# Performance work log

Measured on AMD Instinct MI355X. Metric: run time of the kernel, lower is better.

## Reference

```python
import jax, jax.numpy as jnp
from jax import lax
import numpy as np

W = 64          # net_width
NITER = 10
THRESH = 1e-3
MSTEP = 1.0


def setup_inputs() -> dict:
    key = jax.random.key(0)
    ks = jax.random.split(key, 10)
    B, Nh, DIM = 8, 16384, 1024
    eye = jnp.eye(W, dtype=jnp.float32)
    return {
        'y_re': jax.random.normal(ks[0], (B, 1, Nh), jnp.float32),
        'y_im': jax.random.normal(ks[1], (B, 1, Nh), jnp.float32),
        'H_re': jax.random.normal(ks[2], (32768, DIM), jnp.float32) / np.sqrt(DIM),
        'H_im': jax.random.normal(ks[3], (32768, DIM), jnp.float32) / np.sqrt(DIM),
        # torch inits: estep.weight=I, estep.bias=0, update.weight=I, memory.weight=1e-6*I;
        # add small perturbations so the math is non-degenerate.
        'estep_w': eye + 0.05 * jax.random.normal(ks[4], (W, W), jnp.float32),
        'estep_b': jnp.zeros((W,), jnp.float32),
        'update_w': eye + 0.05 * jax.random.normal(ks[5], (W, W), jnp.float32),
        'update_b': 0.02 * jax.random.normal(ks[6], (W,), jnp.float32),
        'memory_w': 1e-6 * eye + 0.01 * jax.random.normal(ks[7], (W, W), jnp.float32),
        'memory_b': 0.02 * jax.random.normal(ks[8], (W,), jnp.float32),
    }


def _forward(y_re, y_im, H_re, H_im, estep_w, estep_b, update_w, update_b, memory_w, memory_b):
    y = (y_re + 1j * y_im).astype(jnp.complex64)          # [B,1,Nh]
    y = jnp.concatenate([y, jnp.conj(y)], axis=2)         # [B,1,N]
    H = (H_re + 1j * H_im).astype(jnp.complex64)          # [N,DIM]
    B, N = y.shape[0], y.shape[2]
    DIM = H.shape[1]
    nb = N // W
    Hb = H.reshape(nb, W, DIM)                            # [nb,W,DIM]
    yb = y.reshape(B, nb, W).transpose(1, 0, 2)[:, :, None, :]  # [nb,B,1,W]

    x0 = jnp.zeros((B, 1, DIM), jnp.complex64)
    tau0 = jnp.ones((nb, B, 1, W), jnp.float32)

    def block_step(xk, blk):
        H_i, y_i, tau_i = blk                              # [W,DIM], [B,1,W], [B,1,W]
        zk = jnp.einsum('bod,wd->bow', xk, H_i)            # [B,1,W] complex
        r = y_i - zk
        a2 = jnp.abs(r) ** 2                               # [B,1,W] float32
        # expectation_step: xt / std(xt) (torch.std = unbiased, global)
        xt = a2 / jnp.std(a2, ddof=1)
        ht = jax.nn.sigmoid(xt @ estep_w.T + estep_b)
        tau_new = jax.nn.relu(ht @ update_w.T + update_b + tau_i @ memory_w.T + memory_b)
        sigma2 = jnp.mean(a2, axis=2, keepdims=True)       # [B,1,1]
        residual = MSTEP * r * tau_new / sigma2            # complex
        xk = xk + jnp.einsum('bow,wd->bod', residual, jnp.conj(H_i)) / (W * DIM)
        return xk, tau_new

    def iteration(carry, _):
        xk, tau = carry
        xk, tau_new = lax.scan(block_step, xk, (Hb, yb, tau))  # sequential over blocks
        # soft threshold: sgn(x) * relu(|x| - threshold * max|x|)
        ax = jnp.abs(xk)
        m = jnp.max(ax)
        sgn = jnp.where(ax > 0, xk / jnp.where(ax > 0, ax, 1.0), 0.0 + 0.0j)
        xk = sgn * jax.nn.relu(ax - THRESH * m)
        return (xk, tau_new), None

    (xk, tau), _ = lax.scan(iteration, (x0, tau0), None, length=NITER)
    tau_out = tau[:, :, 0, :].transpose(1, 0, 2)           # [B,nb,W]
    return jnp.real(xk), tau_out


def reference(y_re, y_im, H_re, H_im, estep_w, estep_b, update_w, update_b, memory_w, memory_b):
    return _forward(y_re, y_im, H_re, H_im, estep_w, estep_b,
                    update_w, update_b, memory_w, memory_b)
```

## Files before the change

### kernel.cpp

```cpp
#include <hip/hip_runtime.h>
#include <math.h>

#define NT  256
#define NWG 64
#define SCOPE_AG __HIP_MEMORY_SCOPE_AGENT
typedef unsigned long long ull;

__device__ __forceinline__ float ld_f(const float* p) {
    return __hip_atomic_load(p, __ATOMIC_RELAXED, SCOPE_AG);
}
__device__ __forceinline__ void st_f(float* p, float v) {
    __hip_atomic_store(p, v, __ATOMIC_RELAXED, SCOPE_AG);
}
__device__ __forceinline__ unsigned ld_u(const unsigned* p) {
    return __hip_atomic_load(p, __ATOMIC_RELAXED, SCOPE_AG);
}
__device__ __forceinline__ void st_u(unsigned* p, unsigned v) {
    __hip_atomic_store(p, v, __ATOMIC_RELAXED, SCOPE_AG);
}
__device__ __forceinline__ void st_u_rel(unsigned* p, unsigned v) {
    __hip_atomic_store(p, v, __ATOMIC_RELEASE, SCOPE_AG);
}
__device__ __forceinline__ ull ld_u64(const ull* p) {
    return __hip_atomic_load(p, __ATOMIC_RELAXED, SCOPE_AG);
}
__device__ __forceinline__ void st_u64(ull* p, ull v) {
    __hip_atomic_store(p, v, __ATOMIC_RELAXED, SCOPE_AG);
}

__device__ __forceinline__ unsigned tagf(float v, unsigned tg) {
    return (__float_as_uint(v) & 0xFFFFFF00u) | tg;
}
__device__ __forceinline__ ull pack2(float lo, float hi, unsigned tg) {
    return ((ull)tagf(hi, tg) << 32) | (ull)tagf(lo, tg);
}

__device__ __forceinline__ float wsum64(float v) {
    #pragma unroll
    for (int m = 1; m < 64; m <<= 1) v += __shfl_xor(v, m);
    return v;
}
__device__ __forceinline__ float wmax64(float v) {
    #pragma unroll
    for (int m = 1; m < 64; m <<= 1) v = fmaxf(v, __shfl_xor(v, m));
    return v;
}


__launch_bounds__(NT, 1)
__global__ void robii_kernel(
    const float* __restrict__ y_re, const float* __restrict__ y_im,
    const float* __restrict__ H_re, const float* __restrict__ H_im,
    const float* __restrict__ estep_w, const float* __restrict__ estep_b,
    const float* __restrict__ update_w, const float* __restrict__ update_b,
    const float* __restrict__ memory_w, const float* __restrict__ memory_b,
    float* __restrict__ out, float* __restrict__ ws)
{
    __shared__ float wTe[4096], wTu[4096], wTm[4096];
    __shared__ float be[64], bu[64], bm[64];
    __shared__ float a2s[512];
    __shared__ float redl[8];
    __shared__ float gmax[1];
    __shared__ float2 rown[64];
    __shared__ float xts[64], hts[64], taurow[64];
    __shared__ float2 resid[64];
    __shared__ float2 cpartC[4][32][4];
    __shared__ float2 x_l[128];

    float* mpartf = (float*)cpartC;

    const int g = blockIdx.x, t = threadIdx.x;
    const int c = g & 7;
    const int b = g >> 3;
    const int lane = t & 63, wv = t >> 6;
    const int sub = t & 31;
    const int rbase = t >> 5;

    ull*      partuw = (ull*)ws;
    float*    tauws  = ws + 16384;
    unsigned* pm_u   = (unsigned*)(ws + 278528);

    for (int i = t; i < 4096; i += NT) {
        int j = i >> 6, k = i & 63;
        wTe[k * 64 + j] = estep_w[i];
        wTu[k * 64 + j] = update_w[i];
        wTm[k * 64 + j] = memory_w[i];
    }
    if (t < 64) { be[t] = estep_b[t]; bu[t] = update_b[t]; bm[t] = memory_b[t]; taurow[t] = 1.0f; }
    if (t < 128) x_l[t] = make_float2(0.0f, 0.0f);
    for (int i = t; i < 4096; i += NT) st_f(&tauws[g * 4096 + i], 1.0f);

    __syncthreads();
    if (t == 0) st_u_rel(&pm_u[g], tagf(1.0f, 255u));
    if (t < 64) {
        while ((ld_u(&pm_u[t]) & 0xFFu) != 255u) __builtin_amdgcn_s_sleep(1);
    }
    __builtin_amdgcn_fence(__ATOMIC_ACQUIRE, "agent");
    __syncthreads();

    const size_t hcol = (size_t)c * 128 + (size_t)sub * 4;

    float4 hAre[8], hAim[8], hBre[8], hBim[8];

#define PREF(DRE, DIM_, BLKN) do {                                                   \
        const float* _pr = H_re + ((size_t)(BLKN) * 64 + rbase) * 1024 + hcol;       \
        const float* _pi = H_im + ((size_t)(BLKN) * 64 + rbase) * 1024 + hcol;       \
        _Pragma("unroll")                                                            \
        for (int _j = 0; _j < 8; ++_j) {                                             \
            DRE[_j]  = *(const float4*)(_pr + (size_t)_j * 8192);                    \
            DIM_[_j] = *(const float4*)(_pi + (size_t)_j * 8192);                    \
        }                                                                            \
    } while (0)

    PREF(hAre, hAim, 0);

#define STEP(BLK, CRE, CIM, NRE, NIM) do {                                           \
        const int blk = (BLK);                                                       \
        const int par = blk & 1;                                                     \
        const unsigned tg = (unsigned)(iter * 512 + blk + 1) & 0xFFu;                \
        __syncthreads();                               \
           \
               \
        float2 xr0 = x_l[sub * 4 + 0], xr1 = x_l[sub * 4 + 1];                       \
        float2 xr2 = x_l[sub * 4 + 2], xr3 = x_l[sub * 4 + 3];                       \
        _Pragma("unroll")                                                            \
        for (int j = 0; j < 8; ++j) {                                                \
            float4 hr = CRE[j], hi = CIM[j];                                         \
            float sr, si;                                                            \
            sr  = xr0.x * hr.x - xr0.y * hi.x;  si  = xr0.x * hi.x + xr0.y * hr.x;   \
            sr += xr1.x * hr.y - xr1.y * hi.y;  si += xr1.x * hi.y + xr1.y * hr.y;   \
            sr += xr2.x * hr.z - xr2.y * hi.z;  si += xr2.x * hi.z + xr2.y * hr.z;   \
            sr += xr3.x * hr.w - xr3.y * hi.w;  si += xr3.x * hi.w + xr3.y * hr.w;   \
            _Pragma("unroll")                                                        \
            for (int m = 1; m < 32; m <<= 1) {                                       \
                sr += __shfl_xor(sr, m); si += __shfl_xor(si, m);                    \
            }                                                                        \
            if (sub == 0)                                                            \
                st_u64(&partuw[(size_t)par * 4096 + (b * 64 + rbase + 8 * j) * 8 + c], \
                       pack2(sr, si, tg));                                           \
        }                                                                            \
                     \
        PREF(NRE, NIM, ((blk + 1) & 511));                                           \
        float tau_nxt = 0.0f;                                                        \
        if (t < 64) tau_nxt = ld_f(&tauws[(((blk + 1) & 511) * 8 + b) * 64 + t]);    \
        float yAr, yAi, yBr, yBi;                                                    \
        {                                                                            \
            int b1 = t >> 6, w1 = t & 63, n1 = blk * 64 + w1;                        \
            if (n1 < 16384) { yAr = y_re[b1 * 16384 + n1];         yAi = y_im[b1 * 16384 + n1]; } \
            else            { yAr = y_re[b1 * 16384 + n1 - 16384]; yAi = -y_im[b1 * 16384 + n1 - 16384]; } \
            int i2 = t + 256;                                                        \
            int b2 = i2 >> 6, w2 = i2 & 63, n2 = blk * 64 + w2;                      \
            if (n2 < 16384) { yBr = y_re[b2 * 16384 + n2];         yBi = y_im[b2 * 16384 + n2]; } \
            else            { yBr = y_re[b2 * 16384 + n2 - 16384]; yBi = -y_im[b2 * 16384 + n2 - 16384]; } \
        }                                                                            \
         \
        _Pragma("unroll")                                                            \
        for (int e = 0; e < 2; ++e) {                                                \
            int idx = t + e * 256;                                                   \
            const ull* pb = partuw + (size_t)par * 4096 + (size_t)idx * 8;           \
            ull v0, v1, v2, v3, v4, v5, v6, v7;                                      \
            bool ok = false;                                                         \
            while (!ok) {                                                            \
                v0 = ld_u64(pb + 0); v1 = ld_u64(pb + 1);                            \
                v2 = ld_u64(pb + 2); v3 = ld_u64(pb + 3);                            \
                v4 = ld_u64(pb + 4); v5 = ld_u64(pb + 5);                            \
                v6 = ld_u64(pb + 6); v7 = ld_u64(pb + 7);                            \
                unsigned m01 = ((unsigned)v0 & 0xFFu) ^ tg;                          \
                m01 |= ((unsigned)(v0 >> 32) & 0xFFu) ^ tg;                          \
                m01 |= ((unsigned)v1 & 0xFFu) ^ tg;                                  \
                m01 |= ((unsigned)(v1 >> 32) & 0xFFu) ^ tg;                          \
                m01 |= ((unsigned)v2 & 0xFFu) ^ tg;                                  \
                m01 |= ((unsigned)(v2 >> 32) & 0xFFu) ^ tg;                          \
                m01 |= ((unsigned)v3 & 0xFFu) ^ tg;                                  \
                m01 |= ((unsigned)(v3 >> 32) & 0xFFu) ^ tg;                          \
                m01 |= ((unsigned)v4 & 0xFFu) ^ tg;                                  \
                m01 |= ((unsigned)(v4 >> 32) & 0xFFu) ^ tg;                          \
                m01 |= ((unsigned)v5 & 0xFFu) ^ tg;                                  \
                m01 |= ((unsigned)(v5 >> 32) & 0xFFu) ^ tg;                          \
                m01 |= ((unsigned)v6 & 0xFFu) ^ tg;                                  \
                m01 |= ((unsigned)(v6 >> 32) & 0xFFu) ^ tg;                          \
                m01 |= ((unsigned)v7 & 0xFFu) ^ tg;                                  \
                m01 |= ((unsigned)(v7 >> 32) & 0xFFu) ^ tg;                          \
                ok = (m01 == 0u);                                                    \
                if (!ok) __builtin_amdgcn_s_sleep(1);                                \
            }                                                                        \
            float zr = __uint_as_float((unsigned)v0) + __uint_as_float((unsigned)v1) \
                     + __uint_as_float((unsigned)v2) + __uint_as_float((unsigned)v3) \
                     + __uint_as_float((unsigned)v4) + __uint_as_float((unsigned)v5) \
                     + __uint_as_float((unsigned)v6) + __uint_as_float((unsigned)v7);\
            float zi = __uint_as_float((unsigned)(v0 >> 32)) + __uint_as_float((unsigned)(v1 >> 32)) \
                     + __uint_as_float((unsigned)(v2 >> 32)) + __uint_as_float((unsigned)(v3 >> 32)) \
                     + __uint_as_float((unsigned)(v4 >> 32)) + __uint_as_float((unsigned)(v5 >> 32)) \
                     + __uint_as_float((unsigned)(v6 >> 32)) + __uint_as_float((unsigned)(v7 >> 32));\
            float rr = ((e == 0) ? yAr : yBr) - zr;                                  \
            float ri = ((e == 0) ? yAi : yBi) - zi;                                  \
            a2s[idx] = rr * rr + ri * ri;                                            \
            int b1 = idx >> 6, w = idx & 63;                                         \
            if (b1 == b) rown[w] = make_float2(rr, ri);                              \
        }                                                                            \
        __syncthreads();                                                             \
                                       \
        float va = a2s[t] + a2s[t + 256];                                            \
        float s_ = wsum64(va);                                                       \
        if (lane == 0) redl[wv] = s_;                                                \
        __syncthreads();                                                             \
        float mean = (redl[0] + redl[1] + redl[2] + redl[3]) * (1.0f / 512.0f);      \
        float d0 = a2s[t] - mean, d1 = a2s[t + 256] - mean;                          \
        float s2_ = wsum64(d0 * d0 + d1 * d1);                                       \
        float sg  = wsum64(a2s[b * 64 + lane]) * (1.0f / 64.0f);                     \
        if (lane == 0) redl[4 + wv] = s2_;                                           \
        __syncthreads();                                                             \
        float stdv = sqrtf((redl[4] + redl[5] + redl[6] + redl[7]) * (1.0f / 511.0f)); \
        if (t < 64) xts[t] = a2s[b * 64 + t] / stdv;                                 \
        __syncthreads();                                                             \
                                \
        {                                                                            \
            int j = t & 63, q = t >> 6;                                              \
            float acc = 0.0f;                                                        \
            _Pragma("unroll")                                                        \
            for (int k16 = 0; k16 < 16; ++k16) {                                     \
                int k = q * 16 + k16;                                                \
                acc += wTe[k * 64 + j] * xts[k];                                     \
            }                                                                        \
            mpartf[q * 64 + j] = acc;                                                \
        }                                                                            \
        __syncthreads();                                                             \
        if (t < 64) {                                                                \
            float acc = be[t] + mpartf[t] + mpartf[64 + t] + mpartf[128 + t] + mpartf[192 + t]; \
            hts[t] = 1.0f / (1.0f + expf(-acc));                                     \
        }                                                                            \
        __syncthreads();                                                             \
                          \
        {                                                                            \
            int j = t & 63, q = t >> 6;                                              \
            float acc = 0.0f;                                                        \
            _Pragma("unroll")                                                        \
            for (int k16 = 0; k16 < 16; ++k16) {                                     \
                int k = q * 16 + k16;                                                \
                acc += wTu[k * 64 + j] * hts[k] + wTm[k * 64 + j] * taurow[k];       \
            }                                                                        \
            mpartf[q * 64 + j] = acc;                                                \
        }                                                                            \
        __syncthreads();                                                             \
        if (t < 64) {                                                                \
            float tn = bu[t] + bm[t] + mpartf[t] + mpartf[64 + t] + mpartf[128 + t] + mpartf[192 + t]; \
            tn = fmaxf(tn, 0.0f);                                                    \
            if (c == 0) st_f(&tauws[(blk * 8 + b) * 64 + t], tn);                    \
            float2 rv = rown[t];                                                     \
            float scl = tn / sg;                                                     \
            resid[t] = make_float2(rv.x * scl, rv.y * scl);                          \
        }                                                                            \
        __syncthreads();                                                             \
            \
        float2 ac0 = make_float2(0.f, 0.f), ac1 = make_float2(0.f, 0.f);             \
        float2 ac2 = make_float2(0.f, 0.f), ac3 = make_float2(0.f, 0.f);             \
        _Pragma("unroll")                                                            \
        for (int j = 0; j < 8; ++j) {                                                \
            float2 rs = resid[rbase + 8 * j];                                        \
            float4 hr = CRE[j], hi = CIM[j];                                         \
            ac0.x += rs.x * hr.x + rs.y * hi.x;  ac0.y += rs.y * hr.x - rs.x * hi.x; \
            ac1.x += rs.x * hr.y + rs.y * hi.y;  ac1.y += rs.y * hr.y - rs.x * hi.y; \
            ac2.x += rs.x * hr.z + rs.y * hi.z;  ac2.y += rs.y * hr.z - rs.x * hi.z; \
            ac3.x += rs.x * hr.w + rs.y * hi.w;  ac3.y += rs.y * hr.w - rs.x * hi.w; \
        }                                                                            \
        ac0.x += __shfl_xor(ac0.x, 32); ac0.y += __shfl_xor(ac0.y, 32);              \
        ac1.x += __shfl_xor(ac1.x, 32); ac1.y += __shfl_xor(ac1.y, 32);              \
        ac2.x += __shfl_xor(ac2.x, 32); ac2.y += __shfl_xor(ac2.y, 32);              \
        ac3.x += __shfl_xor(ac3.x, 32); ac3.y += __shfl_xor(ac3.y, 32);              \
        if ((t & 32) == 0) {                                                         \
            cpartC[wv][sub][0] = ac0; cpartC[wv][sub][1] = ac1;                      \
            cpartC[wv][sub][2] = ac2; cpartC[wv][sub][3] = ac3;                      \
        }                                                                            \
        if (t < 64) taurow[t] = tau_nxt;                  \
        __syncthreads();                                                             \
        if (t < 128) {                                                               \
            int sl = t >> 2, kk = t & 3;                                             \
            float2 s0 = cpartC[0][sl][kk], s1 = cpartC[1][sl][kk];                   \
            float2 s2 = cpartC[2][sl][kk], s3 = cpartC[3][sl][kk];                   \
            float2 xv = x_l[t];                                                      \
            xv.x += (s0.x + s1.x + s2.x + s3.x) * (1.0f / 65536.0f);                 \
            xv.y += (s0.y + s1.y + s2.y + s3.y) * (1.0f / 65536.0f);                 \
            x_l[t] = xv;                                                             \
        }                                                                            \
    } while (0)

    #pragma unroll 1
    for (int iter = 0; iter < 10; ++iter) {
        #pragma unroll 1
        for (int blk2 = 0; blk2 < 512; blk2 += 2) {
            STEP(blk2,     hAre, hAim, hBre, hBim);
            STEP(blk2 + 1, hBre, hBim, hAre, hAim);
        }

        const unsigned itg = (unsigned)(iter + 1);
        float lm = 0.0f;
        if (t < 128) { float2 xv = x_l[t]; lm = sqrtf(xv.x * xv.x + xv.y * xv.y); }
        lm = wmax64(lm);
        if (lane == 0) redl[wv] = lm;
        __syncthreads();
        if (t == 0)
            st_u_rel(&pm_u[g], tagf(fmaxf(fmaxf(redl[0], redl[1]), fmaxf(redl[2], redl[3])), itg));
        float pv = 0.0f;
        if (t < 64) {
            unsigned u;
            for (;;) {
                u = ld_u(&pm_u[t]);
                if ((u & 0xFFu) == itg) break;
                __builtin_amdgcn_s_sleep(1);
            }
            pv = __uint_as_float(u);
        }
        __builtin_amdgcn_fence(__ATOMIC_ACQUIRE, "agent");
        pv = wmax64(pv);
        if (t == 0) gmax[0] = pv;
        __syncthreads();
        float m = gmax[0];
        if (t < 128) {
            float2 xv = x_l[t];
            float ax = sqrtf(xv.x * xv.x + xv.y * xv.y);
            float s = (ax > 0.0f) ? fmaxf(ax - 1e-3f * m, 0.0f) / ax : 0.0f;
            x_l[t] = make_float2(xv.x * s, xv.y * s);
        }
        __syncthreads();
    }

    if (t < 128) out[b * 1024 + c * 128 + t] = x_l[t].x;
    for (int i = g * 8; i < g * 8 + 8; ++i) {
        for (int idx = t; idx < 512; idx += NT) {
            int bb = idx >> 6, w = idx & 63;
            out[8192 + bb * 32768 + i * 64 + w] = ld_f(&tauws[(i * 8 + bb) * 64 + w]);
        }
    }
#undef STEP
#undef PREF
}

__global__ void robii_diag_kernel(float* out, int code) {
    int i = blockIdx.x * blockDim.x + threadIdx.x;
    if (i < 8192) out[i] = 1.0e6f * (float)(1 + code);
}

extern "C" void kernel_launch(void* const* d_in, const int* in_sizes, int n_in,
                              void* d_out, int out_size, void* d_ws, size_t ws_size,
                              hipStream_t stream) {
    (void)in_sizes; (void)n_in; (void)out_size; (void)ws_size;
    const float* y_re     = (const float*)d_in[0];
    const float* y_im     = (const float*)d_in[1];
    const float* H_re     = (const float*)d_in[2];
    const float* H_im     = (const float*)d_in[3];
    const float* estep_w  = (const float*)d_in[4];
    const float* estep_b  = (const float*)d_in[5];
    const float* update_w = (const float*)d_in[6];
    const float* update_b = (const float*)d_in[7];
    const float* memory_w = (const float*)d_in[8];
    const float* memory_b = (const float*)d_in[9];
    float* outp = (float*)d_out;
    float* wsp  = (float*)d_ws;

    hipLaunchKernelGGL(robii_kernel, dim3(NWG), dim3(NT), 0, stream,
                       y_re, y_im, H_re, H_im, estep_w, estep_b,
                       update_w, update_b, memory_w, memory_b, outp, wsp);
    hipError_t e = hipGetLastError();
    if (e != hipSuccess) {
        hipLaunchKernelGGL(robii_diag_kernel, dim3(32), dim3(256), 0, stream,
                           outp, (int)e);
    }
}
```

Measured before the change: 37.74 ms.

## Process block pairs per step using precomputed bf16 cross-block Gram matrices

```diff
diff --git a/kernel.cpp b/kernel.cpp
--- a/kernel.cpp
+++ b/kernel.cpp
@@ -15,9 +15,6 @@
 __device__ __forceinline__ unsigned ld_u(const unsigned* p) {
     return __hip_atomic_load(p, __ATOMIC_RELAXED, SCOPE_AG);
 }
-__device__ __forceinline__ void st_u(unsigned* p, unsigned v) {
-    __hip_atomic_store(p, v, __ATOMIC_RELAXED, SCOPE_AG);
-}
 __device__ __forceinline__ void st_u_rel(unsigned* p, unsigned v) {
     __hip_atomic_store(p, v, __ATOMIC_RELEASE, SCOPE_AG);
 }
@@ -34,6 +31,13 @@
 __device__ __forceinline__ ull pack2(float lo, float hi, unsigned tg) {
     return ((ull)tagf(hi, tg) << 32) | (ull)tagf(lo, tg);
 }
+__device__ __forceinline__ unsigned bf16pack(float even, float odd) {
+    unsigned ua = __float_as_uint(even); ua += 0x7FFFu + ((ua >> 16) & 1u);
+    unsigned ub = __float_as_uint(odd);  ub += 0x7FFFu + ((ub >> 16) & 1u);
+    return (ua >> 16) | (ub & 0xFFFF0000u);
+}
+__device__ __forceinline__ float bf16lo(unsigned w) { return __uint_as_float(w << 16); }
+__device__ __forceinline__ float bf16hi(unsigned w) { return __uint_as_float(w & 0xFFFF0000u); }
 
 __device__ __forceinline__ float wsum64(float v) {
     #pragma unroll
@@ -46,9 +50,402 @@
     return v;
 }
 
+#define GRAM_WS_BYTES 5374208ull
+#define PART_OFF 1048576
+#define TAU_OFF  1081344
+#define PM_OFF   1343488
+
+__launch_bounds__(256, 1)
+__global__ void gram_kernel(const float* __restrict__ H_re, const float* __restrict__ H_im,
+                            unsigned* __restrict__ Ttab) {
+    __shared__ float2 Als[64 * 65];
+    __shared__ float2 Bls[64 * 65];
+    const int i = blockIdx.x;
+    const int t = threadIdx.x;
+    const int w = t & 63;
+    const int wp0 = (t >> 6) * 16;
+    const size_t baseA = (size_t)(2 * i) * 65536;
+    const size_t baseB = baseA + 65536;
+    float2 acc[16];
+    #pragma unroll
+    for (int s = 0; s < 16; ++s) acc[s] = make_float2(0.0f, 0.0f);
+
+    for (int ch = 0; ch < 16; ++ch) {
+        __syncthreads();
+        for (int k = t; k < 4096; k += 256) {
+            int r = k >> 6, d = k & 63;
+            size_t off = (size_t)r * 1024 + ch * 64 + d;
+            Als[r * 65 + d] = make_float2(H_re[baseA + off], H_im[baseA + off]);
+            Bls[r * 65 + d] = make_float2(H_re[baseB + off], H_im[baseB + off]);
+        }
+        __syncthreads();
+        #pragma unroll
+        for (int s = 0; s < 16; ++s) {
+            int wp = wp0 + s;
+            float ar = 0.0f, ai = 0.0f;
+            #pragma unroll 8
+            for (int d = 0; d < 64; ++d) {
+                float2 a = Als[wp * 65 + d];
+                float2 bb = Bls[w * 65 + d];
+                ar += a.x * bb.x + a.y * bb.y;
+                ai += a.x * bb.y - a.y * bb.x;
+            }
+            acc[s].x += ar; acc[s].y += ai;
+        }
+    }
+    #pragma unroll
+    for (int s = 0; s < 16; ++s)
+        Ttab[(size_t)i * 4096 + w * 64 + (wp0 + s)] = bf16pack(acc[s].x, acc[s].y);
+}
 
 __launch_bounds__(NT, 1)
-__global__ void robii_kernel(
+__global__ void robii_gram(
+    const float* __restrict__ y_re, const float* __restrict__ y_im,
+    const float* __restrict__ H_re, const float* __restrict__ H_im,
+    const float* __restrict__ estep_w, const float* __restrict__ estep_b,
+    const float* __restrict__ update_w, const float* __restrict__ update_b,
+    const float* __restrict__ memory_w, const float* __restrict__ memory_b,
+    float* __restrict__ out, float* __restrict__ ws)
+{
+    __shared__ float wTe[4096], wTu[4096], wTm[4096];
+    __shared__ float be[64], bu[64], bm[64];
+    __shared__ float a2s[512], xts[512], htl[512];
+    __shared__ float redl[8], sgls[8], gmax[1];
+    __shared__ float tauls[1024];
+    __shared__ float2 resA[512], resB[512];
+    __shared__ unsigned Tls[4160];
+    __shared__ float2 cpartC[4][32][4];
+    __shared__ float2 x_l[128];
+
+    const int g = blockIdx.x, t = threadIdx.x;
+    const int c = g & 7;
+    const int b = g >> 3;
+    const int lane = t & 63, wv = t >> 6;
+    const int sub = t & 31;
+    const int rbase = t >> 5;
+
+    unsigned* Ttab  = (unsigned*)ws;
+    ull*      partuw = (ull*)(ws + PART_OFF);
+    float*    tauws  = ws + TAU_OFF;
+    unsigned* pm_u   = (unsigned*)(ws + PM_OFF);
+
+    for (int i = t; i < 4096; i += NT) {
+        int j = i >> 6, k = i & 63;
+        wTe[k * 64 + j] = estep_w[i];
+        wTu[k * 64 + j] = update_w[i];
+        wTm[k * 64 + j] = memory_w[i];
+    }
+    if (t < 64) { be[t] = estep_b[t]; bu[t] = update_b[t]; bm[t] = memory_b[t]; }
+    if (t < 128) x_l[t] = make_float2(0.0f, 0.0f);
+    for (int i = t; i < 1024; i += NT) tauls[i] = 1.0f;
+    for (int i = t; i < 4096; i += NT) st_f(&tauws[g * 4096 + i], 1.0f);
+
+    __syncthreads();
+    if (t == 0) st_u_rel(&pm_u[g], tagf(1.0f, 255u));
+    if (t < 64) {
+        while ((ld_u(&pm_u[t]) & 0xFFu) != 255u) __builtin_amdgcn_s_sleep(1);
+    }
+    __builtin_amdgcn_fence(__ATOMIC_ACQUIRE, "agent");
+    __syncthreads();
+
+    const size_t hcol = (size_t)c * 128 + (size_t)sub * 4;
+    float4 hAre[8], hAim[8], hBre[8], hBim[8];
+    float4 hCre[8], hCim[8], hDre[8], hDim[8];
+
+#define PREF(DRE, DIM_, BLKN) do {                                                   \
+        const float* _pr = H_re + ((size_t)(BLKN) * 64 + rbase) * 1024 + hcol;       \
+        const float* _pi = H_im + ((size_t)(BLKN) * 64 + rbase) * 1024 + hcol;       \
+        _Pragma("unroll")                                                            \
+        for (int _j = 0; _j < 8; ++_j) {                                             \
+            DRE[_j]  = *(const float4*)(_pr + (size_t)_j * 8192);                    \
+            DIM_[_j] = *(const float4*)(_pi + (size_t)_j * 8192);                    \
+        }                                                                            \
+    } while (0)
+
+    PREF(hAre, hAim, 0);
+    PREF(hBre, hBim, 1);
+
+#define TCHK(V) (((((unsigned)(V)) & 0xFFu) ^ tg) | ((((unsigned)((V) >> 32)) & 0xFFu) ^ tg))
+
+#define WSTEP(WN, PRE_, PIM_, QRE_, QIM_, NRE_, NIM_, N2RE_, N2IM_) do {             \
+        const int wn_ = (WN);                                                        \
+        const int par = wn_ & 1;                                                     \
+        const int K0 = 2 * wn_;                                                      \
+        const unsigned tg = (unsigned)(iter * 256 + wn_) & 0xFFu;                    \
+        __syncthreads();                                                             \
+            \
+        float2 xr0 = x_l[sub * 4 + 0], xr1 = x_l[sub * 4 + 1];                       \
+        float2 xr2 = x_l[sub * 4 + 2], xr3 = x_l[sub * 4 + 3];                       \
+        _Pragma("unroll")                                                            \
+        for (int j = 0; j < 8; ++j) {                                                \
+            float4 pr = PRE_[j], pi = PIM_[j], qr = QRE_[j], qi = QIM_[j];           \
+            float sr, si, ur, ui;                                                    \
+            sr  = xr0.x*pr.x - xr0.y*pi.x;  si  = xr0.x*pi.x + xr0.y*pr.x;           \
+            sr += xr1.x*pr.y - xr1.y*pi.y;  si += xr1.x*pi.y + xr1.y*pr.y;           \
+            sr += xr2.x*pr.z - xr2.y*pi.z;  si += xr2.x*pi.z + xr2.y*pr.z;           \
+            sr += xr3.x*pr.w - xr3.y*pi.w;  si += xr3.x*pi.w + xr3.y*pr.w;           \
+            ur  = xr0.x*qr.x - xr0.y*qi.x;  ui  = xr0.x*qi.x + xr0.y*qr.x;           \
+            ur += xr1.x*qr.y - xr1.y*qi.y;  ui += xr1.x*qi.y + xr1.y*qr.y;           \
+            ur += xr2.x*qr.z - xr2.y*qi.z;  ui += xr2.x*qi.z + xr2.y*qr.z;           \
+            ur += xr3.x*qr.w - xr3.y*qi.w;  ui += xr3.x*qi.w + xr3.y*qr.w;           \
+            _Pragma("unroll")                                                        \
+            for (int m = 1; m < 32; m <<= 1) {                                       \
+                sr += __shfl_xor(sr, m); si += __shfl_xor(si, m);                    \
+                ur += __shfl_xor(ur, m); ui += __shfl_xor(ui, m);                    \
+            }                                                                        \
+            int row = b * 64 + rbase + 8 * j;                                        \
+            if (sub == 0)                                                            \
+                st_u64(&partuw[((size_t)(par * 2 + 0) * 512 + row) * 8 + c],         \
+                       pack2(sr, si, tg));                                           \
+            else if (sub == 1)                                                       \
+                st_u64(&partuw[((size_t)(par * 2 + 1) * 512 + row) * 8 + c],         \
+                       pack2(ur, ui, tg));                                           \
+        }                                                                            \
+         \
+        int nb0 = (K0 + 2) & 511, nb1 = (K0 + 3) & 511;                              \
+        PREF(NRE_, NIM_, nb0);                                                       \
+        PREF(N2RE_, N2IM_, nb1);                                                     \
+        for (int q = t; q < 4096; q += NT)                                           \
+            Tls[(q >> 6) * 65 + (q & 63)] = Ttab[(size_t)wn_ * 4096 + q];            \
+        float tnA0 = ld_f(&tauws[nb0 * 512 + t]);                                    \
+        float tnA1 = ld_f(&tauws[nb0 * 512 + t + 256]);                              \
+        float tnB0 = ld_f(&tauws[nb1 * 512 + t]);                                    \
+        float tnB1 = ld_f(&tauws[nb1 * 512 + t + 256]);                              \
+        float y0r[2], y0i[2], y1r[2], y1i[2];                                        \
+        _Pragma("unroll")                                                            \
+        for (int e = 0; e < 2; ++e) {                                                \
+            int idx = t + e * 256; int bb = idx >> 6, w = idx & 63;                  \
+            int n0 = K0 * 64 + w, n1 = n0 + 64;                                      \
+            if (n0 < 16384) { y0r[e] = y_re[bb*16384+n0];       y0i[e] = y_im[bb*16384+n0]; } \
+            else            { y0r[e] = y_re[bb*16384+n0-16384]; y0i[e] = -y_im[bb*16384+n0-16384]; } \
+            if (n1 < 16384) { y1r[e] = y_re[bb*16384+n1];       y1i[e] = y_im[bb*16384+n1]; } \
+            else            { y1r[e] = y_re[bb*16384+n1-16384]; y1i[e] = -y_im[bb*16384+n1-16384]; } \
+        }                                                                            \
+                 \
+        float zpr[2], zpi[2], rr_[2], ri_[2];                                        \
+        _Pragma("unroll")                                                            \
+        for (int e = 0; e < 2; ++e) {                                                \
+            int idx = t + e * 256;                                                   \
+            const ull* p0 = partuw + ((size_t)(par * 2 + 0) * 512 + idx) * 8;        \
+            const ull* p1 = partuw + ((size_t)(par * 2 + 1) * 512 + idx) * 8;        \
+            ull v0,v1,v2,v3,v4,v5,v6,v7,u0,u1,u2,u3,u4,u5,u6,u7;                     \
+            bool ok = false;                                                         \
+            while (!ok) {                                                            \
+                v0=ld_u64(p0+0); v1=ld_u64(p0+1); v2=ld_u64(p0+2); v3=ld_u64(p0+3);  \
+                v4=ld_u64(p0+4); v5=ld_u64(p0+5); v6=ld_u64(p0+6); v7=ld_u64(p0+7);  \
+                u0=ld_u64(p1+0); u1=ld_u64(p1+1); u2=ld_u64(p1+2); u3=ld_u64(p1+3);  \
+                u4=ld_u64(p1+4); u5=ld_u64(p1+5); u6=ld_u64(p1+6); u7=ld_u64(p1+7);  \
+                unsigned mm = TCHK(v0)|TCHK(v1)|TCHK(v2)|TCHK(v3)                    \
+                            | TCHK(v4)|TCHK(v5)|TCHK(v6)|TCHK(v7)                    \
+                            | TCHK(u0)|TCHK(u1)|TCHK(u2)|TCHK(u3)                    \
+                            | TCHK(u4)|TCHK(u5)|TCHK(u6)|TCHK(u7);                   \
+                ok = (mm == 0u);                                                     \
+                if (!ok) __builtin_amdgcn_s_sleep(1);                                \
+            }                                                                        \
+            float zr = __uint_as_float((unsigned)v0) + __uint_as_float((unsigned)v1) \
+                     + __uint_as_float((unsigned)v2) + __uint_as_float((unsigned)v3) \
+                     + __uint_as_float((unsigned)v4) + __uint_as_float((unsigned)v5) \
+                     + __uint_as_float((unsigned)v6) + __uint_as_float((unsigned)v7);\
+            float zi = __uint_as_float((unsigned)(v0>>32)) + __uint_as_float((unsigned)(v1>>32)) \
+                     + __uint_as_float((unsigned)(v2>>32)) + __uint_as_float((unsigned)(v3>>32)) \
+                     + __uint_as_float((unsigned)(v4>>32)) + __uint_as_float((unsigned)(v5>>32)) \
+                     + __uint_as_float((unsigned)(v6>>32)) + __uint_as_float((unsigned)(v7>>32));\
+            zpr[e] = __uint_as_float((unsigned)u0) + __uint_as_float((unsigned)u1)   \
+                   + __uint_as_float((unsigned)u2) + __uint_as_float((unsigned)u3)   \
+                   + __uint_as_float((unsigned)u4) + __uint_as_float((unsigned)u5)   \
+                   + __uint_as_float((unsigned)u6) + __uint_as_float((unsigned)u7);  \
+            zpi[e] = __uint_as_float((unsigned)(u0>>32)) + __uint_as_float((unsigned)(u1>>32)) \
+                   + __uint_as_float((unsigned)(u2>>32)) + __uint_as_float((unsigned)(u3>>32)) \
+                   + __uint_as_float((unsigned)(u4>>32)) + __uint_as_float((unsigned)(u5>>32)) \
+                   + __uint_as_float((unsigned)(u6>>32)) + __uint_as_float((unsigned)(u7>>32));\
+            rr_[e] = y0r[e] - zr; ri_[e] = y0i[e] - zi;                              \
+            a2s[idx] = rr_[e] * rr_[e] + ri_[e] * ri_[e];                            \
+        }                                                                            \
+                     \
+        __syncthreads();                                                             \
+        { float s_ = wsum64(a2s[t] + a2s[t + 256]);                                  \
+          if (lane == 0) redl[wv] = s_; }                                            \
+        __syncthreads();                                                             \
+        { float mean = (redl[0]+redl[1]+redl[2]+redl[3]) * (1.0f/512.0f);            \
+          float d0 = a2s[t]-mean, d1 = a2s[t+256]-mean;                              \
+          float s2_ = wsum64(d0*d0 + d1*d1);                                         \
+          float sgA = wsum64(a2s[wv*64 + lane]);                                     \
+          float sgB = wsum64(a2s[(wv+4)*64 + lane]);                                 \
+          if (lane == 0) { redl[4+wv] = s2_;                                         \
+              sgls[wv] = sgA*(1.0f/64.0f); sgls[wv+4] = sgB*(1.0f/64.0f); } }        \
+        __syncthreads();                                                             \
+        { float stdv = sqrtf((redl[4]+redl[5]+redl[6]+redl[7]) * (1.0f/511.0f));     \
+          xts[t] = a2s[t]/stdv; xts[t+256] = a2s[t+256]/stdv; }                      \
+        __syncthreads();                                                             \
+        _Pragma("unroll")                                                            \
+        for (int e = 0; e < 2; ++e) {                                                \
+            int idx = t + e*256; int bb = idx >> 6, j = idx & 63;                    \
+            float acc = be[j];                                                       \
+            _Pragma("unroll")                                                        \
+            for (int k = 0; k < 64; ++k) acc += wTe[k*64+j] * xts[bb*64+k];          \
+            htl[idx] = 1.0f/(1.0f+expf(-acc));                                       \
+        }                                                                            \
+        __syncthreads();                                                             \
+        _Pragma("unroll")                                                            \
+        for (int e = 0; e < 2; ++e) {                                                \
+            int idx = t + e*256; int bb = idx >> 6, j = idx & 63;                    \
+            float acc = bu[j] + bm[j];                                               \
+            _Pragma("unroll")                                                        \
+            for (int k = 0; k < 64; ++k)                                             \
+                acc += wTu[k*64+j]*htl[bb*64+k] + wTm[k*64+j]*tauls[bb*64+k];        \
+            float tn = fmaxf(acc, 0.0f);                                             \
+            if (c == 0 && bb == b) st_f(&tauws[(size_t)K0 * 512 + idx], tn);         \
+            float scl = tn / sgls[bb];                                               \
+            resA[idx] = make_float2(rr_[e]*scl, ri_[e]*scl);                         \
+        }                                                                            \
+        __syncthreads();                                                             \
+              \
+        _Pragma("unroll")                                                            \
+        for (int e = 0; e < 2; ++e) {                                                \
+            int idx = t + e*256; int bb = idx >> 6, w = idx & 63;                    \
+            float cr = 0.0f, ci = 0.0f;                                              \
+            _Pragma("unroll 8")                                                      \
+            for (int wp = 0; wp < 64; ++wp) {                                        \
+                float2 rs = resA[bb*64 + wp];                                        \
+                unsigned gw = Tls[w*65 + wp];                                        \
+                float gr = bf16lo(gw), gi = bf16hi(gw);                              \
+                cr += rs.x*gr - rs.y*gi;                                             \
+                ci += rs.x*gi + rs.y*gr;                                             \
+            }                                                                        \
+            float z1r = zpr[e] + cr * (1.0f/65536.0f);                               \
+            float z1i = zpi[e] + ci * (1.0f/65536.0f);                               \
+            rr_[e] = y1r[e] - z1r; ri_[e] = y1i[e] - z1i;                            \
+            a2s[idx] = rr_[e]*rr_[e] + ri_[e]*ri_[e];                                \
+        }                                                                            \
+        __syncthreads();                                                             \
+        { float s_ = wsum64(a2s[t] + a2s[t + 256]);                                  \
+          if (lane == 0) redl[wv] = s_; }                                            \
+        __syncthreads();                                                             \
+        { float mean = (redl[0]+redl[1]+redl[2]+redl[3]) * (1.0f/512.0f);            \
+          float d0 = a2s[t]-mean, d1 = a2s[t+256]-mean;                              \
+          float s2_ = wsum64(d0*d0 + d1*d1);                                         \
+          float sgA = wsum64(a2s[wv*64 + lane]);                                     \
+          float sgB = wsum64(a2s[(wv+4)*64 + lane]);                                 \
+          if (lane == 0) { redl[4+wv] = s2_;                                         \
+              sgls[wv] = sgA*(1.0f/64.0f); sgls[wv+4] = sgB*(1.0f/64.0f); } }        \
+        __syncthreads();                                                             \
+        { float stdv = sqrtf((redl[4]+redl[5]+redl[6]+redl[7]) * (1.0f/511.0f));     \
+          xts[t] = a2s[t]/stdv; xts[t+256] = a2s[t+256]/stdv; }                      \
+        __syncthreads();                                                             \
+        _Pragma("unroll")                                                            \
+        for (int e = 0; e < 2; ++e) {                                                \
+            int idx = t + e*256; int bb = idx >> 6, j = idx & 63;                    \
+            float acc = be[j];                                                       \
+            _Pragma("unroll")                                                        \
+            for (int k = 0; k < 64; ++k) acc += wTe[k*64+j] * xts[bb*64+k];          \
+            htl[idx] = 1.0f/(1.0f+expf(-acc));                                       \
+        }                                                                            \
+        __syncthreads();                                                             \
+        _Pragma("unroll")                                                            \
+        for (int e = 0; e < 2; ++e) {                                                \
+            int idx = t + e*256; int bb = idx >> 6, j = idx & 63;                    \
+            float acc = bu[j] + bm[j];                                               \
+            _Pragma("unroll")                                                        \
+            for (int k = 0; k < 64; ++k)                                             \
+                acc += wTu[k*64+j]*htl[bb*64+k] + wTm[k*64+j]*tauls[512 + bb*64+k];  \
+            float tn = fmaxf(acc, 0.0f);                                             \
+            if (c == 0 && bb == b) st_f(&tauws[(size_t)(K0+1) * 512 + idx], tn);     \
+            float scl = tn / sgls[bb];                                               \
+            resB[idx] = make_float2(rr_[e]*scl, ri_[e]*scl);                         \
+        }                                                                            \
+        __syncthreads();                                                             \
+            \
+        float2 ac0 = make_float2(0.f,0.f), ac1 = make_float2(0.f,0.f);               \
+        float2 ac2 = make_float2(0.f,0.f), ac3 = make_float2(0.f,0.f);               \
+        _Pragma("unroll")                                                            \
+        for (int j = 0; j < 8; ++j) {                                                \
+            float2 ra = resA[b*64 + rbase + 8*j];                                    \
+            float2 rb2 = resB[b*64 + rbase + 8*j];                                   \
+            float4 pr = PRE_[j], pi = PIM_[j], qr = QRE_[j], qi = QIM_[j];           \
+            ac0.x += ra.x*pr.x + ra.y*pi.x + rb2.x*qr.x + rb2.y*qi.x;                \
+            ac0.y += ra.y*pr.x - ra.x*pi.x + rb2.y*qr.x - rb2.x*qi.x;                \
+            ac1.x += ra.x*pr.y + ra.y*pi.y + rb2.x*qr.y + rb2.y*qi.y;                \
+            ac1.y += ra.y*pr.y - ra.x*pi.y + rb2.y*qr.y - rb2.x*qi.y;                \
+            ac2.x += ra.x*pr.z + ra.y*pi.z + rb2.x*qr.z + rb2.y*qi.z;                \
+            ac2.y += ra.y*pr.z - ra.x*pi.z + rb2.y*qr.z - rb2.x*qi.z;                \
+            ac3.x += ra.x*pr.w + ra.y*pi.w + rb2.x*qr.w + rb2.y*qi.w;                \
+            ac3.y += ra.y*pr.w - ra.x*pi.w + rb2.y*qr.w - rb2.x*qi.w;                \
+        }                                                                            \
+        ac0.x += __shfl_xor(ac0.x, 32); ac0.y += __shfl_xor(ac0.y, 32);              \
+        ac1.x += __shfl_xor(ac1.x, 32); ac1.y += __shfl_xor(ac1.y, 32);              \
+        ac2.x += __shfl_xor(ac2.x, 32); ac2.y += __shfl_xor(ac2.y, 32);              \
+        ac3.x += __shfl_xor(ac3.x, 32); ac3.y += __shfl_xor(ac3.y, 32);              \
+        if ((t & 32) == 0) {                                                         \
+            cpartC[wv][sub][0] = ac0; cpartC[wv][sub][1] = ac1;                      \
+            cpartC[wv][sub][2] = ac2; cpartC[wv][sub][3] = ac3;                      \
+        }                                                                            \
+        tauls[t] = tnA0; tauls[t + 256] = tnA1;        \
+        tauls[512 + t] = tnB0; tauls[512 + t + 256] = tnB1;                          \
+        __syncthreads();                                                             \
+        if (t < 128) {                                                               \
+            int sl = t >> 2, kk = t & 3;                                             \
+            float2 s0 = cpartC[0][sl][kk], s1 = cpartC[1][sl][kk];                   \
+            float2 s2 = cpartC[2][sl][kk], s3 = cpartC[3][sl][kk];                   \
+            float2 xv = x_l[t];                                                      \
+            xv.x += (s0.x + s1.x + s2.x + s3.x) * (1.0f/65536.0f);                   \
+            xv.y += (s0.y + s1.y + s2.y + s3.y) * (1.0f/65536.0f);                   \
+            x_l[t] = xv;                                                             \
+        }                                                                            \
+    } while (0)
+
+    #pragma unroll 1
+    for (int iter = 0; iter < 10; ++iter) {
+        #pragma unroll 1
+        for (int wn = 0; wn < 256; wn += 2) {
+            WSTEP(wn,     hAre, hAim, hBre, hBim, hCre, hCim, hDre, hDim);
+            WSTEP(wn + 1, hCre, hCim, hDre, hDim, hAre, hAim, hBre, hBim);
+        }
+        const unsigned itg = (unsigned)(iter + 1);
+        float lm = 0.0f;
+        if (t < 128) { float2 xv = x_l[t]; lm = sqrtf(xv.x*xv.x + xv.y*xv.y); }
+        lm = wmax64(lm);
+        if (lane == 0) redl[wv] = lm;
+        __syncthreads();
+        if (t == 0)
+            st_u_rel(&pm_u[g], tagf(fmaxf(fmaxf(redl[0], redl[1]), fmaxf(redl[2], redl[3])), itg));
+        float pv = 0.0f;
+        if (t < 64) {
+            unsigned u;
+            for (;;) {
+                u = ld_u(&pm_u[t]);
+                if ((u & 0xFFu) == itg) break;
+                __builtin_amdgcn_s_sleep(1);
+            }
+            pv = __uint_as_float(u);
+        }
+        __builtin_amdgcn_fence(__ATOMIC_ACQUIRE, "agent");
+        pv = wmax64(pv);
+        if (t == 0) gmax[0] = pv;
+        __syncthreads();
+        float m = gmax[0];
+        if (t < 128) {
+            float2 xv = x_l[t];
+            float ax = sqrtf(xv.x*xv.x + xv.y*xv.y);
+            float s = (ax > 0.0f) ? fmaxf(ax - 1e-3f * m, 0.0f) / ax : 0.0f;
+            x_l[t] = make_float2(xv.x * s, xv.y * s);
+        }
+        __syncthreads();
+    }
+
+    if (t < 128) out[b * 1024 + c * 128 + t] = x_l[t].x;
+    for (int i = g * 8; i < g * 8 + 8; ++i) {
+        for (int idx = t; idx < 512; idx += NT) {
+            int bb = idx >> 6, w = idx & 63;
+            out[8192 + bb * 32768 + i * 64 + w] = ld_f(&tauws[(size_t)i * 512 + bb * 64 + w]);
+        }
+    }
+#undef WSTEP
+#undef TCHK
+#undef PREF
+}
+
+__launch_bounds__(NT, 1)
+__global__ void robii_fb(
     const float* __restrict__ y_re, const float* __restrict__ y_im,
     const float* __restrict__ H_re, const float* __restrict__ H_im,
     const float* __restrict__ estep_w, const float* __restrict__ estep_b,
@@ -66,7 +463,6 @@
     __shared__ float2 resid[64];
     __shared__ float2 cpartC[4][32][4];
     __shared__ float2 x_l[128];
-
     float* mpartf = (float*)cpartC;
 
     const int g = blockIdx.x, t = threadIdx.x;
@@ -89,7 +485,6 @@
     if (t < 64) { be[t] = estep_b[t]; bu[t] = update_b[t]; bm[t] = memory_b[t]; taurow[t] = 1.0f; }
     if (t < 128) x_l[t] = make_float2(0.0f, 0.0f);
     for (int i = t; i < 4096; i += NT) st_f(&tauws[g * 4096 + i], 1.0f);
-
     __syncthreads();
     if (t == 0) st_u_rel(&pm_u[g], tagf(1.0f, 255u));
     if (t < 64) {
@@ -99,7 +494,6 @@
     __syncthreads();
 
     const size_t hcol = (size_t)c * 128 + (size_t)sub * 4;
-
     float4 hAre[8], hAim[8], hBre[8], hBim[8];
 
 #define PREF(DRE, DIM_, BLKN) do {                                                   \
@@ -118,19 +512,17 @@
         const int blk = (BLK);                                                       \
         const int par = blk & 1;                                                     \
         const unsigned tg = (unsigned)(iter * 512 + blk + 1) & 0xFFu;                \
-        __syncthreads();                               \
-           \
-               \
+        __syncthreads();                                                             \
         float2 xr0 = x_l[sub * 4 + 0], xr1 = x_l[sub * 4 + 1];                       \
         float2 xr2 = x_l[sub * 4 + 2], xr3 = x_l[sub * 4 + 3];                       \
         _Pragma("unroll")                                                            \
         for (int j = 0; j < 8; ++j) {                                                \
             float4 hr = CRE[j], hi = CIM[j];                                         \
             float sr, si;                                                            \
-            sr  = xr0.x * hr.x - xr0.y * hi.x;  si  = xr0.x * hi.x + xr0.y * hr.x;   \
-            sr += xr1.x * hr.y - xr1.y * hi.y;  si += xr1.x * hi.y + xr1.y * hr.y;   \
-            sr += xr2.x * hr.z - xr2.y * hi.z;  si += xr2.x * hi.z + xr2.y * hr.z;   \
-            sr += xr3.x * hr.w - xr3.y * hi.w;  si += xr3.x * hi.w + xr3.y * hr.w;   \
+            sr  = xr0.x*hr.x - xr0.y*hi.x;  si  = xr0.x*hi.x + xr0.y*hr.x;           \
+            sr += xr1.x*hr.y - xr1.y*hi.y;  si += xr1.x*hi.y + xr1.y*hr.y;           \
+            sr += xr2.x*hr.z - xr2.y*hi.z;  si += xr2.x*hi.z + xr2.y*hr.z;           \
+            sr += xr3.x*hr.w - xr3.y*hi.w;  si += xr3.x*hi.w + xr3.y*hr.w;           \
             _Pragma("unroll")                                                        \
             for (int m = 1; m < 32; m <<= 1) {                                       \
                 sr += __shfl_xor(sr, m); si += __shfl_xor(si, m);                    \
@@ -139,21 +531,19 @@
                 st_u64(&partuw[(size_t)par * 4096 + (b * 64 + rbase + 8 * j) * 8 + c], \
                        pack2(sr, si, tg));                                           \
         }                                                                            \
-                     \
         PREF(NRE, NIM, ((blk + 1) & 511));                                           \
         float tau_nxt = 0.0f;                                                        \
         if (t < 64) tau_nxt = ld_f(&tauws[(((blk + 1) & 511) * 8 + b) * 64 + t]);    \
         float yAr, yAi, yBr, yBi;                                                    \
         {                                                                            \
             int b1 = t >> 6, w1 = t & 63, n1 = blk * 64 + w1;                        \
-            if (n1 < 16384) { yAr = y_re[b1 * 16384 + n1];         yAi = y_im[b1 * 16384 + n1]; } \
-            else            { yAr = y_re[b1 * 16384 + n1 - 16384]; yAi = -y_im[b1 * 16384 + n1 - 16384]; } \
+            if (n1 < 16384) { yAr = y_re[b1*16384+n1];       yAi = y_im[b1*16384+n1]; } \
+            else            { yAr = y_re[b1*16384+n1-16384]; yAi = -y_im[b1*16384+n1-16384]; } \
             int i2 = t + 256;                                                        \
             int b2 = i2 >> 6, w2 = i2 & 63, n2 = blk * 64 + w2;                      \
-            if (n2 < 16384) { yBr = y_re[b2 * 16384 + n2];         yBi = y_im[b2 * 16384 + n2]; } \
-            else            { yBr = y_re[b2 * 16384 + n2 - 16384]; yBi = -y_im[b2 * 16384 + n2 - 16384]; } \
-        }                                                                            \
-         \
+            if (n2 < 16384) { yBr = y_re[b2*16384+n2];       yBi = y_im[b2*16384+n2]; } \
+            else            { yBr = y_re[b2*16384+n2-16384]; yBi = -y_im[b2*16384+n2-16384]; } \
+        }                                                                            \
         _Pragma("unroll")                                                            \
         for (int e = 0; e < 2; ++e) {                                                \
             int idx = t + e * 256;                                                   \
@@ -165,22 +555,14 @@
                 v2 = ld_u64(pb + 2); v3 = ld_u64(pb + 3);                            \
                 v4 = ld_u64(pb + 4); v5 = ld_u64(pb + 5);                            \
                 v6 = ld_u64(pb + 6); v7 = ld_u64(pb + 7);                            \
-                unsigned m01 = ((unsigned)v0 & 0xFFu) ^ tg;                          \
-                m01 |= ((unsigned)(v0 >> 32) & 0xFFu) ^ tg;                          \
-                m01 |= ((unsigned)v1 & 0xFFu) ^ tg;                                  \
-                m01 |= ((unsigned)(v1 >> 32) & 0xFFu) ^ tg;                          \
-                m01 |= ((unsigned)v2 & 0xFFu) ^ tg;                                  \
-                m01 |= ((unsigned)(v2 >> 32) & 0xFFu) ^ tg;                          \
-                m01 |= ((unsigned)v3 & 0xFFu) ^ tg;                                  \
-                m01 |= ((unsigned)(v3 >> 32) & 0xFFu) ^ tg;                          \
-                m01 |= ((unsigned)v4 & 0xFFu) ^ tg;                                  \
-                m01 |= ((unsigned)(v4 >> 32) & 0xFFu) ^ tg;                          \
-                m01 |= ((unsigned)v5 & 0xFFu) ^ tg;                                  \
-                m01 |= ((unsigned)(v5 >> 32) & 0xFFu) ^ tg;                          \
-                m01 |= ((unsigned)v6 & 0xFFu) ^ tg;                                  \
-                m01 |= ((unsigned)(v6 >> 32) & 0xFFu) ^ tg;                          \
-                m01 |= ((unsigned)v7 & 0xFFu) ^ tg;                                  \
-                m01 |= ((unsigned)(v7 >> 32) & 0xFFu) ^ tg;                          \
+                unsigned m01 = (((unsigned)v0 & 0xFFu) ^ tg) | ((((unsigned)(v0>>32)) & 0xFFu) ^ tg) \
+                  | (((unsigned)v1 & 0xFFu) ^ tg) | ((((unsigned)(v1>>32)) & 0xFFu) ^ tg) \
+                  | (((unsigned)v2 & 0xFFu) ^ tg) | ((((unsigned)(v2>>32)) & 0xFFu) ^ tg) \
+                  | (((unsigned)v3 & 0xFFu) ^ tg) | ((((unsigned)(v3>>32)) & 0xFFu) ^ tg) \
+                  | (((unsigned)v4 & 0xFFu) ^ tg) | ((((unsigned)(v4>>32)) & 0xFFu) ^ tg) \
+                  | (((unsigned)v5 & 0xFFu) ^ tg) | ((((unsigned)(v5>>32)) & 0xFFu) ^ tg) \
+                  | (((unsigned)v6 & 0xFFu) ^ tg) | ((((unsigned)(v6>>32)) & 0xFFu) ^ tg) \
+                  | (((unsigned)v7 & 0xFFu) ^ tg) | ((((unsigned)(v7>>32)) & 0xFFu) ^ tg); \
                 ok = (m01 == 0u);                                                    \
                 if (!ok) __builtin_amdgcn_s_sleep(1);                                \
             }                                                                        \
@@ -188,10 +570,10 @@
                      + __uint_as_float((unsigned)v2) + __uint_as_float((unsigned)v3) \
                      + __uint_as_float((unsigned)v4) + __uint_as_float((unsigned)v5) \
                      + __uint_as_float((unsigned)v6) + __uint_as_float((unsigned)v7);\
-            float zi = __uint_as_float((unsigned)(v0 >> 32)) + __uint_as_float((unsigned)(v1 >> 32)) \
-                     + __uint_as_float((unsigned)(v2 >> 32)) + __uint_as_float((unsigned)(v3 >> 32)) \
-                     + __uint_as_float((unsigned)(v4 >> 32)) + __uint_as_float((unsigned)(v5 >> 32)) \
-                     + __uint_as_float((unsigned)(v6 >> 32)) + __uint_as_float((unsigned)(v7 >> 32));\
+            float zi = __uint_as_float((unsigned)(v0>>32)) + __uint_as_float((unsigned)(v1>>32)) \
+                     + __uint_as_float((unsigned)(v2>>32)) + __uint_as_float((unsigned)(v3>>32)) \
+                     + __uint_as_float((unsigned)(v4>>32)) + __uint_as_float((unsigned)(v5>>32)) \
+                     + __uint_as_float((unsigned)(v6>>32)) + __uint_as_float((unsigned)(v7>>32));\
             float rr = ((e == 0) ? yAr : yBr) - zr;                                  \
             float ri = ((e == 0) ? yAi : yBi) - zi;                                  \
             a2s[idx] = rr * rr + ri * ri;                                            \
@@ -199,7 +581,6 @@
             if (b1 == b) rown[w] = make_float2(rr, ri);                              \
         }                                                                            \
         __syncthreads();                                                             \
-                                       \
         float va = a2s[t] + a2s[t + 256];                                            \
         float s_ = wsum64(va);                                                       \
         if (lane == 0) redl[wv] = s_;                                                \
@@ -213,7 +594,6 @@
         float stdv = sqrtf((redl[4] + redl[5] + redl[6] + redl[7]) * (1.0f / 511.0f)); \
         if (t < 64) xts[t] = a2s[b * 64 + t] / stdv;                                 \
         __syncthreads();                                                             \
-                                \
         {                                                                            \
             int j = t & 63, q = t >> 6;                                              \
             float acc = 0.0f;                                                        \
@@ -230,7 +610,6 @@
             hts[t] = 1.0f / (1.0f + expf(-acc));                                     \
         }                                                                            \
         __syncthreads();                                                             \
-                          \
         {                                                                            \
             int j = t & 63, q = t >> 6;                                              \
             float acc = 0.0f;                                                        \
@@ -251,17 +630,16 @@
             resid[t] = make_float2(rv.x * scl, rv.y * scl);                          \
         }                                                                            \
         __syncthreads();                                                             \
-            \
         float2 ac0 = make_float2(0.f, 0.f), ac1 = make_float2(0.f, 0.f);             \
         float2 ac2 = make_float2(0.f, 0.f), ac3 = make_float2(0.f, 0.f);             \
         _Pragma("unroll")                                                            \
         for (int j = 0; j < 8; ++j) {                                                \
             float2 rs = resid[rbase + 8 * j];                                        \
             float4 hr = CRE[j], hi = CIM[j];                                         \
-            ac0.x += rs.x * hr.x + rs.y * hi.x;  ac0.y += rs.y * hr.x - rs.x * hi.x; \
-            ac1.x += rs.x * hr.y + rs.y * hi.y;  ac1.y += rs.y * hr.y - rs.x * hi.y; \
-            ac2.x += rs.x * hr.z + rs.y * hi.z;  ac2.y += rs.y * hr.z - rs.x * hi.z; \
-            ac3.x += rs.x * hr.w + rs.y * hi.w;  ac3.y += rs.y * hr.w - rs.x * hi.w; \
+            ac0.x += rs.x*hr.x + rs.y*hi.x;  ac0.y += rs.y*hr.x - rs.x*hi.x;         \
+            ac1.x += rs.x*hr.y + rs.y*hi.y;  ac1.y += rs.y*hr.y - rs.x*hi.y;         \
+            ac2.x += rs.x*hr.z + rs.y*hi.z;  ac2.y += rs.y*hr.z - rs.x*hi.z;         \
+            ac3.x += rs.x*hr.w + rs.y*hi.w;  ac3.y += rs.y*hr.w - rs.x*hi.w;         \
         }                                                                            \
         ac0.x += __shfl_xor(ac0.x, 32); ac0.y += __shfl_xor(ac0.y, 32);              \
         ac1.x += __shfl_xor(ac1.x, 32); ac1.y += __shfl_xor(ac1.y, 32);              \
@@ -271,7 +649,7 @@
             cpartC[wv][sub][0] = ac0; cpartC[wv][sub][1] = ac1;                      \
             cpartC[wv][sub][2] = ac2; cpartC[wv][sub][3] = ac3;                      \
         }                                                                            \
-        if (t < 64) taurow[t] = tau_nxt;                  \
+        if (t < 64) taurow[t] = tau_nxt;                                             \
         __syncthreads();                                                             \
         if (t < 128) {                                                               \
             int sl = t >> 2, kk = t & 3;                                             \
@@ -291,10 +669,9 @@
             STEP(blk2,     hAre, hAim, hBre, hBim);
             STEP(blk2 + 1, hBre, hBim, hAre, hAim);
         }
-
         const unsigned itg = (unsigned)(iter + 1);
         float lm = 0.0f;
-        if (t < 128) { float2 xv = x_l[t]; lm = sqrtf(xv.x * xv.x + xv.y * xv.y); }
+        if (t < 128) { float2 xv = x_l[t]; lm = sqrtf(xv.x*xv.x + xv.y*xv.y); }
         lm = wmax64(lm);
         if (lane == 0) redl[wv] = lm;
         __syncthreads();
@@ -317,7 +694,7 @@
         float m = gmax[0];
         if (t < 128) {
             float2 xv = x_l[t];
-            float ax = sqrtf(xv.x * xv.x + xv.y * xv.y);
+            float ax = sqrtf(xv.x*xv.x + xv.y*xv.y);
             float s = (ax > 0.0f) ? fmaxf(ax - 1e-3f * m, 0.0f) / ax : 0.0f;
             x_l[t] = make_float2(xv.x * s, xv.y * s);
         }
@@ -343,7 +720,7 @@
 extern "C" void kernel_launch(void* const* d_in, const int* in_sizes, int n_in,
                               void* d_out, int out_size, void* d_ws, size_t ws_size,
                               hipStream_t stream) {
-    (void)in_sizes; (void)n_in; (void)out_size; (void)ws_size;
+    (void)in_sizes; (void)n_in; (void)out_size;
     const float* y_re     = (const float*)d_in[0];
     const float* y_im     = (const float*)d_in[1];
     const float* H_re     = (const float*)d_in[2];
@@ -357,9 +734,17 @@
     float* outp = (float*)d_out;
     float* wsp  = (float*)d_ws;
 
-    hipLaunchKernelGGL(robii_kernel, dim3(NWG), dim3(NT), 0, stream,
-                       y_re, y_im, H_re, H_im, estep_w, estep_b,
-                       update_w, update_b, memory_w, memory_b, outp, wsp);
+    if (ws_size >= GRAM_WS_BYTES) {
+        hipLaunchKernelGGL(gram_kernel, dim3(256), dim3(256), 0, stream,
+                           H_re, H_im, (unsigned*)wsp);
+        hipLaunchKernelGGL(robii_gram, dim3(NWG), dim3(NT), 0, stream,
+                           y_re, y_im, H_re, H_im, estep_w, estep_b,
+                           update_w, update_b, memory_w, memory_b, outp, wsp);
+    } else {
+        hipLaunchKernelGGL(robii_fb, dim3(NWG), dim3(NT), 0, stream,
+                           y_re, y_im, H_re, H_im, estep_w, estep_b,
+                           update_w, update_b, memory_w, memory_b, outp, wsp);
+    }
     hipError_t e = hipGetLastError();
     if (e != hipSuccess) {
         hipLaunchKernelGGL(robii_diag_kernel, dim3(32), dim3(256), 0, stream,
```

After: 101.7 ms. 169% more time.
